# Performance work log

Hardware: AMD Instinct MI355X
Metric: run time of the kernel (lower is better)

## Reference

```python
import jax, jax.numpy as jnp
import numpy as np
from functools import partial

EPS = 1e-5
CHANS = [(3, 64), (64, 64), (64, 128), (128, 128), (128, 256), (256, 256), (256, 256), (256, 256)]

def conv3d(x, w):
    # x: [B,X,Y,Z,Cin], w: [3,3,3,Cin,Cout]; Minkowski stride-1 conv keeps coords -> SAME padding
    return jax.lax.conv_general_dilated(x, w, window_strides=(1, 1, 1), padding='SAME',
                                        dimension_numbers=('NDHWC', 'DHWIO', 'NDHWC'))

def bn(x, g, b):
    # training-mode batch norm over all voxels (MinkowskiBatchNorm forward)
    m = jnp.mean(x, axis=(0, 1, 2, 3))
    v = jnp.var(x, axis=(0, 1, 2, 3))
    return (x - m) * jax.lax.rsqrt(v + EPS) * g + b

def maxpool2(x):
    return jax.lax.reduce_window(x, -jnp.inf, jax.lax.max,
                                 (1, 2, 2, 2, 1), (1, 2, 2, 2, 1), 'VALID')

def setup_inputs() -> dict:
    key = jax.random.key(0)
    ks = jax.random.split(key, 32)
    inp = {'x': jax.random.normal(ks[0], (2, 64, 64, 64, 3), dtype=jnp.float32)}
    for i, (ci, co) in enumerate(CHANS):
        scale = (2.0 / (27 * ci)) ** 0.5  # kaiming for 3x3x3 conv
        inp[f'w{i+1}'] = jax.random.normal(ks[1 + i], (3, 3, 3, ci, co), dtype=jnp.float32) * scale
        inp[f'g{i+1}'] = jnp.ones((co,), dtype=jnp.float32)
        inp[f'b{i+1}'] = jnp.zeros((co,), dtype=jnp.float32)
    inp['wl'] = jax.random.normal(ks[20], (256, 256), dtype=jnp.float32) * (1.0 / 16.0)
    inp['bl'] = jnp.zeros((256,), dtype=jnp.float32)
    return inp

def reference(x, w1, g1, b1, w2, g2, b2, w3, g3, b3, w4, g4, b4,
              w5, g5, b5, w6, g6, b6, w7, g7, b7, w8, g8, b8, wl, bl):
    h = jax.nn.relu(bn(conv3d(x, w1), g1, b1))
    h = jax.nn.relu(bn(conv3d(h, w2), g2, b2))
    h = maxpool2(h)                                   # 64 -> 32
    h = jax.nn.relu(bn(conv3d(h, w3), g3, b3))
    h = jax.nn.relu(bn(conv3d(h, w4), g4, b4))
    h = maxpool2(h)                                   # 32 -> 16
    h = jax.nn.relu(bn(conv3d(h, w5), g5, b5))
    h = jax.nn.relu(bn(conv3d(h, w6), g6, b6))
    h = jax.nn.relu(bn(conv3d(h, w7), g7, b7))
    h = maxpool2(h)                                   # 16 -> 8
    h = bn(conv3d(h, w8), g8, b8)                     # no ReLU before global pool in source
    h = jnp.mean(h, axis=(1, 2, 3))                   # MinkowskiGlobalPooling (avg over coords)
    return h @ wl + bl                                # MinkowskiLinear(256, out_feat)
```

## Files before the change

kernel.cpp:

```cpp
#include <hip/hip_runtime.h>


typedef _Float16 f16;
typedef _Float16 f16x8 __attribute__((ext_vector_type(8)));
typedef _Float16 f16x4 __attribute__((ext_vector_type(4)));
typedef float f32x4 __attribute__((ext_vector_type(4)));

__device__ __forceinline__ int xcd_swz(int bx, int nbx) {
  const int q = nbx >> 3, r = nbx & 7;
  const int x = bx & 7, o = bx >> 3;
  return (x < r ? x * (q + 1) : r * (q + 1) + (x - r) * q) + o;
}

struct WArgs {
  const float* src[8];
  int end[8];
  int S[8], G[8], CR[8], CO[8];
};
__global__ __launch_bounds__(256) void wprep_all(WArgs a, f16* __restrict__ wf)
{
  const int e = blockIdx.x * 256 + threadIdx.x;
  int li = 0;
  while (li < 7 && e >= a.end[li]) ++li;
  if (e >= a.end[li]) return;
  const int base = li ? a.end[li - 1] : 0;
  int x = e - base;
  const int i = x & 7;
  const int l = (x >> 3) & 63;
  int r = x >> 9;
  const int g = r % a.G[li]; r /= a.G[li];
  const int s = r % a.S[li]; r /= a.S[li];
  const int t = r;
  const int k = s * 32 + ((l >> 4) << 3) + i;
  const int co = g * 16 + (l & 15);
  float v;
  if (li == 0) {
    const int tap = k >> 3, ci = k & 7;
    v = (ci < 3 && tap < 27) ? a.src[0][((long)tap * 3 + ci) * 64 + co] : 0.f;
  } else {
    v = (k < a.CR[li]) ? a.src[li][((long)t * a.CR[li] + k) * a.CO[li] + co] : 0.f;
  }
  wf[e] = (f16)v;
}

__global__ __launch_bounds__(256) void conv1_mfma(
    const float* __restrict__ xin, const f16* __restrict__ wf,
    f16* __restrict__ out, float* __restrict__ part)
{
  constexpr int Z = 64, Y = 64, X = 64, L = 4;
  constexpr int RB = 48;
  constexpr int SLAB = (L + 2) * (Z + 2) * RB;
  __shared__ __align__(16) char slab[3 * SLAB];
  __shared__ float sstat[4][2][64];

  const int tid = threadIdx.x;
  const int lane = tid & 63;
  const int wr = tid >> 6;

  const int bxs = xcd_swz(blockIdx.x, gridDim.x);
  const long vb = (long)bxs * 256;
  const int n = (int)(vb >> 18);
  const int rem = (int)(vb & 262143);
  const int x0 = rem >> 12;
  const int y0 = (rem >> 6) & 63;

  if (tid < 36) {
    const int s = tid / 12, pr = tid % 12;
    const int row = (pr >> 1) * (Z + 2) + (pr & 1) * (Z + 1);
    const f16x8 hz = {};
    *(f16x8*)(slab + s * SLAB + row * RB) = hz;
  }

  for (int rr2 = tid; rr2 < 3 * (L + 2) * Z; rr2 += 256) {
    const int s = rr2 / ((L + 2) * Z);
    const int rr = rr2 % ((L + 2) * Z);
    const int li = rr / Z, z = rr % Z;
    const int xs = x0 + s - 1, ys = y0 - 1 + li;
    f16x8 h = {};
    if (xs >= 0 && xs < X && ys >= 0 && ys < Y) {
      const float* p = xin + (((long)(n * X + xs) * Y + ys) * Z + z) * 3;
      h[0] = (f16)p[0]; h[1] = (f16)p[1]; h[2] = (f16)p[2];
    }
    *(f16x8*)(slab + s * SLAB + (li * (Z + 2) + 1 + z) * RB) = h;
  }

  int abase[4];
  #pragma unroll
  for (int r = 0; r < 4; ++r) {
    const int vl = wr * 64 + r * 16 + (lane & 15);
    abase[r] = ((vl >> 6) * (Z + 2) + (vl & 63)) * RB;
  }
  const int c = lane >> 4;
  int rofftab[7];
  #pragma unroll
  for (int j = 0; j < 7; ++j) {
    const int tap = 4 * j + c;
    if (tap < 27) {
      const int dx = tap / 9, dy = (tap / 3) % 3, dz = tap % 3;
      rofftab[j] = dx * SLAB + (dy * (Z + 2) + dz) * RB;
    } else {
      rofftab[j] = 0;
    }
  }

  f32x4 acc[4][4];
  const f32x4 fz = {0.f, 0.f, 0.f, 0.f};
  #pragma unroll
  for (int r = 0; r < 4; ++r)
    #pragma unroll
    for (int cc = 0; cc < 4; ++cc) acc[r][cc] = fz;

  __syncthreads();

  #pragma unroll
  for (int j = 0; j < 7; ++j) {
    f16x8 av[4];
    #pragma unroll
    for (int r = 0; r < 4; ++r)
      av[r] = *(const f16x8*)(slab + abase[r] + rofftab[j]);
    f16x8 bv[4];
    #pragma unroll
    for (int c2 = 0; c2 < 4; ++c2)
      bv[c2] = *(const f16x8*)((const char*)wf + ((j * 4 + c2) << 10) + (lane << 4));
    #pragma unroll
    for (int r = 0; r < 4; ++r)
      #pragma unroll
      for (int c2 = 0; c2 < 4; ++c2)
        acc[r][c2] = __builtin_amdgcn_mfma_f32_16x16x32_f16(av[r], bv[c2], acc[r][c2], 0, 0, 0);
  }

  const long vgbase = vb + wr * 64;
  #pragma unroll
  for (int r = 0; r < 4; ++r)
    #pragma unroll
    for (int cc = 0; cc < 4; ++cc)
      #pragma unroll
      for (int q = 0; q < 4; ++q) {
        const long vox = vgbase + r * 16 + ((lane >> 4) << 2) + q;
        const int co = cc * 16 + (lane & 15);
        out[vox * 64 + co] = (f16)acc[r][cc][q];
      }

  float s4[4], q4[4];
  #pragma unroll
  for (int cc = 0; cc < 4; ++cc) {
    float s = 0.f, q = 0.f;
    #pragma unroll
    for (int r = 0; r < 4; ++r)
      #pragma unroll
      for (int qd = 0; qd < 4; ++qd) {
        const float v = acc[r][cc][qd];
        s += v;
        q = fmaf(v, v, q);
      }
    s4[cc] = s; q4[cc] = q;
  }
  #pragma unroll
  for (int cc = 0; cc < 4; ++cc) {
    s4[cc] += __shfl_xor(s4[cc], 16);
    s4[cc] += __shfl_xor(s4[cc], 32);
    q4[cc] += __shfl_xor(q4[cc], 16);
    q4[cc] += __shfl_xor(q4[cc], 32);
  }
  if (lane < 16) {
    #pragma unroll
    for (int cc = 0; cc < 4; ++cc) {
      sstat[wr][0][cc * 16 + lane] = s4[cc];
      sstat[wr][1][cc * 16 + lane] = q4[cc];
    }
  }
  __syncthreads();
  for (int t = tid; t < 128; t += 256) {
    const int k = (t >> 6) & 1, ch = t & 63;
    float v = 0.f;
    #pragma unroll
    for (int w2 = 0; w2 < 4; ++w2) v += sstat[w2][k][ch];
    part[(long)bxs * 128 + k * 64 + ch] = v;
  }
}

template<int CIN, int Z, int WR, int WC, bool HASBN, int SS>
__global__ __launch_bounds__(WR*WC*64) void conv_mfma(
    const f16* __restrict__ xin, const f16* __restrict__ wf,
    f16* __restrict__ out, int X, int Y, int Co,
    const float* __restrict__ sc, const float* __restrict__ sh,
    float* __restrict__ part, int partBase,
    float* __restrict__ pout, long outE)
{
  constexpr int NTHR = WR * WC * 64;
  constexpr int L = 64 * WR / Z;
  constexpr int RB = CIN * 2;
  constexpr int S = CIN / 32;
  constexpr int COW = 64 * WC;
  constexpr bool SPLIT = (SS > 0);
  __shared__ __align__(16) char slab[(L + 2) * (Z + 2) * RB];
  __shared__ float sstat[SPLIT ? 1 : WR * WC][2][64];

  const int tid = threadIdx.x;
  const int lane = tid & 63;
  const int wv = tid >> 6;
  const int wr = wv / WC, wc = wv % WC;

  const int bxs = xcd_swz(blockIdx.x, gridDim.x);
  const long vb = (long)bxs * (64 * WR);
  const int XYZ = X * Y * Z;
  const int n = (int)(vb / XYZ);
  const int rem = (int)(vb % XYZ);
  const int x0 = rem / (Y * Z);
  const int y0 = (rem % (Y * Z)) / Z;
  const int co0 = blockIdx.y * COW;
  const int Gtot = Co >> 4;
  const int g0 = (co0 >> 4) + wc * 4;

  int arow[4];
  #pragma unroll
  for (int r = 0; r < 4; ++r) {
    const int vl = wr * 64 + r * 16 + (lane & 15);
    arow[r] = (vl / Z) * (Z + 2) + (vl % Z);
  }
  const int kbyte = (lane >> 4) << 4;

  f32x4 acc[4][4];
  const f32x4 fz = {0.f, 0.f, 0.f, 0.f};
  #pragma unroll
  for (int r = 0; r < 4; ++r)
    #pragma unroll
    for (int c = 0; c < 4; ++c) acc[r][c] = fz;

  {
    const f16x8 hz = {};
    for (int e = tid * 8; e < (L + 2) * 2 * CIN; e += NTHR * 8) {
      const int pr = e / CIN, ci = e % CIN;
      const int row = (pr >> 1) * (Z + 2) + (pr & 1) * (Z + 1);
      *(f16x8*)(slab + row * RB + ((ci * 2) ^ ((row & 7) << 4))) = hz;
    }
  }

  auto stage = [&](int dx) {
    const int xs = x0 + dx - 1;
    const bool xok = (xs >= 0) && (xs < X);
    const long gv0 = ((long)(n * X + xs) * Y + (y0 - 1)) * Z;
    constexpr int NE = (L + 2) * Z * CIN;
    for (int e = tid * 8; e < NE; e += NTHR * 8) {
      const int rr = e / CIN, ci = e % CIN;
      const int li = rr / Z, z = rr % Z;
      const int ys = y0 - 1 + li;
      f16x8 h = {};
      if (xok && ys >= 0 && ys < Y) {
        h = *(const f16x8*)(xin + (gv0 + rr) * CIN + ci);
        if constexpr (HASBN) {
          const float4 s0 = *(const float4*)(sc + ci);
          const float4 s1 = *(const float4*)(sc + ci + 4);
          const float4 h0 = *(const float4*)(sh + ci);
          const float4 h1 = *(const float4*)(sh + ci + 4);
          h[0] = (f16)fmaxf(fmaf((float)h[0], s0.x, h0.x), 0.f);
          h[1] = (f16)fmaxf(fmaf((float)h[1], s0.y, h0.y), 0.f);
          h[2] = (f16)fmaxf(fmaf((float)h[2], s0.z, h0.z), 0.f);
          h[3] = (f16)fmaxf(fmaf((float)h[3], s0.w, h0.w), 0.f);
          h[4] = (f16)fmaxf(fmaf((float)h[4], s1.x, h1.x), 0.f);
          h[5] = (f16)fmaxf(fmaf((float)h[5], s1.y, h1.y), 0.f);
          h[6] = (f16)fmaxf(fmaf((float)h[6], s1.z, h1.z), 0.f);
          h[7] = (f16)fmaxf(fmaf((float)h[7], s1.w, h1.w), 0.f);
        }
      }
      const int row = li * (Z + 2) + 1 + z;
      *(f16x8*)(slab + row * RB + ((ci * 2) ^ ((row & 7) << 4))) = h;
    }
  };

  auto ktaps = [&](int dx, int s) {
    #pragma unroll
    for (int dy = 0; dy < 3; ++dy) {
      #pragma unroll
      for (int dzi = 0; dzi < 3; ++dzi) {
        f16x8 av[4];
        #pragma unroll
        for (int r = 0; r < 4; ++r) {
          const int row = arow[r] + dy * (Z + 2) + dzi;
          av[r] = *(const f16x8*)(slab + row * RB +
                    ((s * 64 + kbyte) ^ ((row & 7) << 4)));
        }
        const int t = dx * 9 + dy * 3 + dzi;
        f16x8 bv[4];
        #pragma unroll
        for (int c = 0; c < 4; ++c)
          bv[c] = *(const f16x8*)((const char*)wf +
                    (((long)(t * S + s) * Gtot + g0 + c) << 10) + (lane << 4));
        #pragma unroll
        for (int r = 0; r < 4; ++r)
          #pragma unroll
          for (int c = 0; c < 4; ++c)
            acc[r][c] = __builtin_amdgcn_mfma_f32_16x16x32_f16(av[r], bv[c], acc[r][c], 0, 0, 0);
      }
    }
  };

  if constexpr (SPLIT) {
    constexpr int SCH = S / SS;
    const int zb = blockIdx.z;
    const int dx = zb / SS;
    const int s0 = (zb % SS) * SCH;
    stage(dx);
    __syncthreads();
    #pragma unroll
    for (int si = 0; si < SCH; ++si) ktaps(dx, s0 + si);
  } else {
    for (int dx = 0; dx < 3; ++dx) {
      __syncthreads();
      stage(dx);
      __syncthreads();
      for (int s = 0; s < S; ++s) ktaps(dx, s);
    }
  }

  const long vgbase = vb + wr * 64;
  const int cobase = co0 + wc * 64;
  if constexpr (SPLIT) {
    float* pb = pout + (long)blockIdx.z * outE;
    #pragma unroll
    for (int r = 0; r < 4; ++r)
      #pragma unroll
      for (int c = 0; c < 4; ++c)
        #pragma unroll
        for (int q = 0; q < 4; ++q) {
          const long vox = vgbase + r * 16 + ((lane >> 4) << 2) + q;
          const int co = cobase + c * 16 + (lane & 15);
          pb[vox * Co + co] = acc[r][c][q];
        }
    return;
  }

  #pragma unroll
  for (int r = 0; r < 4; ++r)
    #pragma unroll
    for (int c = 0; c < 4; ++c)
      #pragma unroll
      for (int q = 0; q < 4; ++q) {
        const long vox = vgbase + r * 16 + ((lane >> 4) << 2) + q;
        const int co = cobase + c * 16 + (lane & 15);
        out[vox * Co + co] = (f16)acc[r][c][q];
      }

  float s4[4], q4[4];
  #pragma unroll
  for (int c = 0; c < 4; ++c) {
    float s = 0.f, q = 0.f;
    #pragma unroll
    for (int r = 0; r < 4; ++r)
      #pragma unroll
      for (int qd = 0; qd < 4; ++qd) {
        const float v = acc[r][c][qd];
        s += v;
        q = fmaf(v, v, q);
      }
    s4[c] = s; q4[c] = q;
  }
  #pragma unroll
  for (int c = 0; c < 4; ++c) {
    s4[c] += __shfl_xor(s4[c], 16);
    s4[c] += __shfl_xor(s4[c], 32);
    q4[c] += __shfl_xor(q4[c], 16);
    q4[c] += __shfl_xor(q4[c], 32);
  }
  if (lane < 16) {
    #pragma unroll
    for (int c = 0; c < 4; ++c) {
      sstat[wv][0][c * 16 + lane] = s4[c];
      sstat[wv][1][c * 16 + lane] = q4[c];
    }
  }
  __syncthreads();
  const long entry = (long)blockIdx.y * gridDim.x + bxs + partBase;
  for (int t = tid; t < WC * 128; t += NTHR) {
    const int wcc = t >> 7, k = (t >> 6) & 1, ch = t & 63;
    float v = 0.f;
    #pragma unroll
    for (int wr2 = 0; wr2 < WR; ++wr2) v += sstat[wr2 * WC + wcc][k][ch];
    part[entry * (2 * COW) + k * COW + wcc * 64 + ch] = v;
  }
}

__global__ __launch_bounds__(256) void reduce_stats(
    const float* __restrict__ pout, f16* __restrict__ out,
    long outE, int KS, int vpb, float* __restrict__ part)
{
  const int tid = threadIdx.x;
  const int wv = tid >> 6, lane = tid & 63;
  const int vbase = blockIdx.x * vpb;
  float4 s = {0.f, 0.f, 0.f, 0.f}, q = {0.f, 0.f, 0.f, 0.f};
  for (int v = vbase + wv; v < vbase + vpb; v += 4) {
    const long e = (long)v * 256 + lane * 4;
    float4 o = *(const float4*)(pout + e);
    for (int z = 1; z < KS; ++z) {
      const float4 p = *(const float4*)(pout + (long)z * outE + e);
      o.x += p.x; o.y += p.y; o.z += p.z; o.w += p.w;
    }
    f16x4 ov = {(f16)o.x, (f16)o.y, (f16)o.z, (f16)o.w};
    *(f16x4*)(out + e) = ov;
    s.x += o.x; s.y += o.y; s.z += o.z; s.w += o.w;
    q.x = fmaf(o.x, o.x, q.x); q.y = fmaf(o.y, o.y, q.y);
    q.z = fmaf(o.z, o.z, q.z); q.w = fmaf(o.w, o.w, q.w);
  }
  __shared__ float st[4][2][256];
  *(float4*)&st[wv][0][lane * 4] = s;
  *(float4*)&st[wv][1][lane * 4] = q;
  __syncthreads();
  for (int t = tid; t < 512; t += 256) {
    const int k = t >> 8, ch = t & 255;
    part[(long)blockIdx.x * 512 + k * 256 + ch] =
        st[0][k][ch] + st[1][k][ch] + st[2][k][ch] + st[3][k][ch];
  }
}

__global__ __launch_bounds__(256) void stats_final(
    const float* __restrict__ part, int nbx, int CoWin, long nvox,
    const float* __restrict__ g, const float* __restrict__ b,
    float* __restrict__ sc, float* __restrict__ sh)
{
  const int c = blockIdx.x;
  const int by = c / CoWin;
  const int cw = c % CoWin;
  const int tid = threadIdx.x;
  float s = 0.f, ss = 0.f;
  for (int i = tid; i < nbx; i += 256) {
    const long base = ((long)by * nbx + i) * 2 * CoWin;
    s += part[base + cw];
    ss += part[base + CoWin + cw];
  }
  __shared__ float r0[256];
  __shared__ float r1[256];
  r0[tid] = s; r1[tid] = ss;
  __syncthreads();
  #pragma unroll
  for (int o = 128; o > 0; o >>= 1) {
    if (tid < o) { r0[tid] += r0[tid + o]; r1[tid] += r1[tid + o]; }
    __syncthreads();
  }
  if (tid == 0) {
    const float inv = 1.f / (float)nvox;
    const float m = r0[0] * inv;
    const float var = r1[0] * inv - m * m;
    const float scale = rsqrtf(var + 1e-5f) * g[c];
    sc[c] = scale;
    sh[c] = b[c] - m * scale;
  }
}

__global__ __launch_bounds__(256) void maxpool2_aff(
    const f16* __restrict__ in, f16* __restrict__ out,
    int N, int X, int Y, int Z, int C,
    const float* __restrict__ sc, const float* __restrict__ sh)
{
  const int OX = X >> 1, OY = Y >> 1, OZ = Z >> 1;
  const int c4n = C >> 2;
  const long nout = (long)N * OX * OY * OZ * c4n;
  long idx = (long)blockIdx.x * 256 + threadIdx.x;
  if (idx >= nout) return;
  const int c4 = (int)(idx % c4n);
  long v = idx / c4n;
  const int oz = (int)(v % OZ); v /= OZ;
  const int oy = (int)(v % OY); v /= OY;
  const int ox = (int)(v % OX);
  const int n = (int)(v / OX);
  const long sx = (long)Y * Z * C, sy = (long)Z * C, sz = C;
  const long base = ((((long)n * X + 2 * ox) * Y + 2 * oy) * Z + 2 * oz) * (long)C + 4L * c4;
  f16x4 m = *(const f16x4*)(in + base);
  #pragma unroll
  for (int dd = 1; dd < 8; ++dd) {
    const int dxp = dd >> 2, dyp = (dd >> 1) & 1, dzp = dd & 1;
    const f16x4 t = *(const f16x4*)(in + base + dxp * sx + dyp * sy + dzp * sz);
    #pragma unroll
    for (int i = 0; i < 4; ++i) m[i] = (t[i] > m[i]) ? t[i] : m[i];
  }
  const int c = 4 * c4;
  const float4 s4 = *(const float4*)(sc + c);
  const float4 h4 = *(const float4*)(sh + c);
  f16x4 r;
  r[0] = (f16)fmaxf(fmaf((float)m[0], s4.x, h4.x), 0.f);
  r[1] = (f16)fmaxf(fmaf((float)m[1], s4.y, h4.y), 0.f);
  r[2] = (f16)fmaxf(fmaf((float)m[2], s4.z, h4.z), 0.f);
  r[3] = (f16)fmaxf(fmaf((float)m[3], s4.w, h4.w), 0.f);
  *(f16x4*)(out + idx * 4) = r;
}

__global__ __launch_bounds__(256) void head_mean(
    const f16* __restrict__ x8, const float* __restrict__ sc, const float* __restrict__ sh,
    float* __restrict__ hbuf)
{
  const int n = blockIdx.x, cg = blockIdx.y;
  const int tx = threadIdx.x & 63, ty = threadIdx.x >> 6;
  const int c = cg * 64 + tx;
  float s = 0.f;
  for (int v = ty; v < 512; v += 4) s += (float)x8[((long)n * 512 + v) * 256 + c];
  __shared__ float red[4][64];
  red[ty][tx] = s;
  __syncthreads();
  if (ty == 0) {
    s = red[0][tx] + red[1][tx] + red[2][tx] + red[3][tx];
    hbuf[n * 256 + c] = fmaf(s * (1.f / 512.f), sc[c], sh[c]);
  }
}

__global__ __launch_bounds__(256) void head_mv(
    const float* __restrict__ hbuf, const float* __restrict__ wl,
    const float* __restrict__ bl, float* __restrict__ out)
{
  const int n = blockIdx.x, og = blockIdx.y;
  const int tx = threadIdx.x & 63, ty = threadIdx.x >> 6;
  const int oc = og * 64 + tx;
  float a = 0.f;
  const int k0 = ty * 64;
  for (int k = k0; k < k0 + 64; ++k)
    a = fmaf(hbuf[n * 256 + k], wl[(long)k * 256 + oc], a);
  __shared__ float red[4][64];
  red[ty][tx] = a;
  __syncthreads();
  if (ty == 0)
    out[n * 256 + oc] = red[0][tx] + red[1][tx] + red[2][tx] + red[3][tx] + bl[oc];
}

extern "C" void kernel_launch(void* const* d_in, const int* in_sizes, int n_in,
                              void* d_out, int out_size, void* d_ws, size_t ws_size,
                              hipStream_t stream)
{
  const float* x = (const float*)d_in[0];
  const float* W[8];
  const float* G[8];
  const float* B[8];
  for (int i = 0; i < 8; ++i) {
    W[i] = (const float*)d_in[1 + 3 * i];
    G[i] = (const float*)d_in[2 + 3 * i];
    B[i] = (const float*)d_in[3 + 3 * i];
  }
  const float* wl = (const float*)d_in[25];
  const float* bl = (const float*)d_in[26];

  char* ws = (char*)d_ws;
  f16*   A    = (f16*)ws;
  f16*   Bb   = (f16*)(ws + (64L << 20));
  float* pK   = (float*)(ws + (128L << 20));
  float* part = (float*)(ws + (152L << 20));
  float* scb  = part + 262144L;
  float* shb  = scb + 2048L;
  float* hbuf = shb + 2048L;
  f16*   wfb  = (f16*)(hbuf + 512L);

  const int wfS[8]  = {7, 2, 2, 4, 4, 8, 8, 8};
  const int wfG[8]  = {4, 4, 8, 8, 16, 16, 16, 16};
  const int wfT[8]  = {1, 27, 27, 27, 27, 27, 27, 27};
  const int wfCR[8] = {3, 64, 64, 128, 128, 256, 256, 256};
  const int wfCO[8] = {64, 64, 128, 128, 256, 256, 256, 256};
  long wfOff[9];
  wfOff[0] = 0;
  for (int i = 0; i < 8; ++i) wfOff[i + 1] = wfOff[i] + (long)wfT[i] * wfS[i] * wfG[i] * 512;
  if (ws_size < (size_t)((char*)(wfb + wfOff[8]) - ws)) return;
  auto WF = [&](int i) { return wfb + wfOff[i]; };
  auto SC = [&](int i) { return scb + i * 256; };
  auto SH = [&](int i) { return shb + i * 256; };

  {
    WArgs a;
    for (int i = 0; i < 8; ++i) {
      a.src[i] = W[i]; a.end[i] = (int)wfOff[i + 1];
      a.S[i] = wfS[i]; a.G[i] = wfG[i]; a.CR[i] = wfCR[i]; a.CO[i] = wfCO[i];
    }
    wprep_all<<<(unsigned)((wfOff[8] + 255) / 256), 256, 0, stream>>>(a, wfb);
  }

  auto fin = [&](int layer, int nbx, int CoWin, int C, long nvox) {
    stats_final<<<C, 256, 0, stream>>>(part, nbx, CoWin, nvox,
                                       G[layer], B[layer], SC(layer), SH(layer));
  };
  auto pool_aff = [&](const f16* in, f16* ob, int N, int Xd, int Yd, int Zd, int C, int layer) {
    const long nout = (long)N * (Xd / 2) * (Yd / 2) * (Zd / 2) * (C / 4);
    maxpool2_aff<<<(unsigned)((nout + 255) / 256), 256, 0, stream>>>(
        in, ob, N, Xd, Yd, Zd, C, SC(layer), SH(layer));
  };

  conv1_mfma<<<2048, 256, 0, stream>>>(x, WF(0), A, part);
  fin(0, 2048, 64, 64, 524288);
  conv_mfma<64, 64, 4, 1, true, 0><<<dim3(2048, 1), 256, 0, stream>>>(
      A, WF(1), Bb, 64, 64, 64, SC(0), SH(0), part, 0, nullptr, 0);
  fin(1, 2048, 64, 64, 524288);
  pool_aff(Bb, A, 2, 64, 64, 64, 64, 1);

  conv_mfma<64, 32, 2, 2, false, 0><<<dim3(512, 1), 256, 0, stream>>>(
      A, WF(2), Bb, 32, 32, 128, nullptr, nullptr, part, 0, nullptr, 0);
  fin(2, 512, 128, 128, 65536);
  conv_mfma<128, 32, 2, 2, true, 0><<<dim3(512, 1), 256, 0, stream>>>(
      Bb, WF(3), A, 32, 32, 128, SC(2), SH(2), part, 0, nullptr, 0);
  fin(3, 512, 128, 128, 65536);
  pool_aff(A, Bb, 2, 32, 32, 32, 128, 3);

  const long E16 = 2097152;
  conv_mfma<128, 16, 1, 4, false, 1><<<dim3(128, 1, 3), 256, 0, stream>>>(
      Bb, WF(4), nullptr, 16, 16, 256, nullptr, nullptr, nullptr, 0, pK, E16);
  reduce_stats<<<256, 256, 0, stream>>>(pK, A, E16, 3, 32, part);
  fin(4, 256, 256, 256, 8192);
  conv_mfma<256, 16, 1, 4, true, 1><<<dim3(128, 1, 3), 256, 0, stream>>>(
      A, WF(5), nullptr, 16, 16, 256, SC(4), SH(4), nullptr, 0, pK, E16);
  reduce_stats<<<256, 256, 0, stream>>>(pK, Bb, E16, 3, 32, part);
  fin(5, 256, 256, 256, 8192);
  conv_mfma<256, 16, 1, 4, true, 1><<<dim3(128, 1, 3), 256, 0, stream>>>(
      Bb, WF(6), nullptr, 16, 16, 256, SC(5), SH(5), nullptr, 0, pK, E16);
  reduce_stats<<<256, 256, 0, stream>>>(pK, A, E16, 3, 32, part);
  fin(6, 256, 256, 256, 8192);
  pool_aff(A, Bb, 2, 16, 16, 16, 256, 6);

  const long E8 = 262144;
  conv_mfma<256, 8, 1, 4, false, 4><<<dim3(16, 1, 12), 256, 0, stream>>>(
      Bb, WF(7), nullptr, 8, 8, 256, nullptr, nullptr, nullptr, 0, pK, E8);
  reduce_stats<<<256, 256, 0, stream>>>(pK, A, E8, 12, 4, part);
  fin(7, 256, 256, 256, 1024);

  head_mean<<<dim3(2, 4), 256, 0, stream>>>(A, SC(7), SH(7), hbuf);
  head_mv<<<dim3(2, 4), 256, 0, stream>>>(hbuf, wl, bl, (float*)d_out);
}
```

Measured before the change: 572.1 us.

## Add double-buffered z-half pipelined conv kernel for non-split layers

Adds a conv_pipe kernel that splits each dx slab into two z-halves, double-buffers them in shared memory, and prefetches the next stage into registers while MFMAs run on the current one. Global loads now overlap with compute instead of serialising behind a barrier between stage and compute. It is used for conv2, conv3 and conv4, and the old conv_mfma is reduced to the split-K path. The cost is more barriers (six stages instead of three), extra halo rows per half, and register pressure from the prefetch buffers.

Result: slower. 728.9 us (+27.4%).

```diff
diff --git a/kernel.cpp b/kernel.cpp
--- a/kernel.cpp
+++ b/kernel.cpp
@@ -179,22 +179,27 @@
   }
 }
 
-template<int CIN, int Z, int WR, int WC, bool HASBN, int SS>
-__global__ __launch_bounds__(WR*WC*64) void conv_mfma(
+template<int CIN, int Z, int WR, int WC, bool HASBN>
+__global__ __launch_bounds__(WR*WC*64) void conv_pipe(
     const f16* __restrict__ xin, const f16* __restrict__ wf,
     f16* __restrict__ out, int X, int Y, int Co,
     const float* __restrict__ sc, const float* __restrict__ sh,
-    float* __restrict__ part, int partBase,
-    float* __restrict__ pout, long outE)
+    float* __restrict__ part, int partBase)
 {
   constexpr int NTHR = WR * WC * 64;
   constexpr int L = 64 * WR / Z;
-  constexpr int RB = CIN * 2;
+  constexpr int ZH = Z / 2;
+  constexpr int ZR = ZH + 2;
+  constexpr int RBB = CIN * 2;
+  constexpr int HROWS = (L + 2) * ZR;
+  constexpr int NE_H = HROWS * CIN;
+  constexpr int NLD = (NE_H + NTHR * 8 - 1) / (NTHR * 8);
+  constexpr int NL2 = (NLD + 1) / 2;
   constexpr int S = CIN / 32;
+  constexpr int SH2 = S / 2;
   constexpr int COW = 64 * WC;
-  constexpr bool SPLIT = (SS > 0);
-  __shared__ __align__(16) char slab[(L + 2) * (Z + 2) * RB];
-  __shared__ float sstat[SPLIT ? 1 : WR * WC][2][64];
+  __shared__ __align__(16) char slab[2][HROWS * RBB];
+  __shared__ float sstat[WR * WC][2][64];
 
   const int tid = threadIdx.x;
   const int lane = tid & 63;
@@ -216,6 +221,209 @@
   #pragma unroll
   for (int r = 0; r < 4; ++r) {
     const int vl = wr * 64 + r * 16 + (lane & 15);
+    arow[r] = (vl / Z) * ZR + ((r * 16) % ZH) + (lane & 15);
+  }
+  const int kbyte = (lane >> 4) << 4;
+
+  f32x4 acc[4][4];
+  const f32x4 fz = {0.f, 0.f, 0.f, 0.f};
+  #pragma unroll
+  for (int r = 0; r < 4; ++r)
+    #pragma unroll
+    for (int c = 0; c < 4; ++c) acc[r][c] = fz;
+
+  f16x8 regs[NL2];
+
+  auto LOADH = [&](int k1, int half) {
+    const int dx = k1 >> 1, zh = k1 & 1;
+    const int xs = x0 + dx - 1;
+    const long gplane = (long)(n * X + xs) * Y;
+    #pragma unroll
+    for (int j = 0; j < NL2; ++j) {
+      const int slot = half * NL2 + j;
+      const int e = tid * 8 + slot * NTHR * 8;
+      f16x8 h = {};
+      if (slot < NLD && e < NE_H) {
+        const int rr = e / CIN, ci = e % CIN;
+        const int li = rr / ZR, zr = rr % ZR;
+        const int ys = y0 - 1 + li;
+        const int zs = zh * ZH - 1 + zr;
+        if (xs >= 0 && xs < X && ys >= 0 && ys < Y && zs >= 0 && zs < Z)
+          h = *(const f16x8*)(xin + ((gplane + ys) * Z + zs) * CIN + ci);
+      }
+      regs[j] = h;
+    }
+  };
+
+  auto WRITEH = [&](int k1, int half) {
+    const int dx = k1 >> 1, zh = k1 & 1;
+    const int xs = x0 + dx - 1;
+    char* buf = slab[k1 & 1];
+    #pragma unroll
+    for (int j = 0; j < NL2; ++j) {
+      const int slot = half * NL2 + j;
+      const int e = tid * 8 + slot * NTHR * 8;
+      if (slot < NLD && e < NE_H) {
+        const int rr = e / CIN, ci = e % CIN;
+        const int li = rr / ZR, zr = rr % ZR;
+        const int ys = y0 - 1 + li;
+        const int zs = zh * ZH - 1 + zr;
+        f16x8 h = regs[j];
+        if constexpr (HASBN) {
+          if (xs >= 0 && xs < X && ys >= 0 && ys < Y && zs >= 0 && zs < Z) {
+            const float4 s0 = *(const float4*)(sc + ci);
+            const float4 s1 = *(const float4*)(sc + ci + 4);
+            const float4 h0 = *(const float4*)(sh + ci);
+            const float4 h1 = *(const float4*)(sh + ci + 4);
+            h[0] = (f16)fmaxf(fmaf((float)h[0], s0.x, h0.x), 0.f);
+            h[1] = (f16)fmaxf(fmaf((float)h[1], s0.y, h0.y), 0.f);
+            h[2] = (f16)fmaxf(fmaf((float)h[2], s0.z, h0.z), 0.f);
+            h[3] = (f16)fmaxf(fmaf((float)h[3], s0.w, h0.w), 0.f);
+            h[4] = (f16)fmaxf(fmaf((float)h[4], s1.x, h1.x), 0.f);
+            h[5] = (f16)fmaxf(fmaf((float)h[5], s1.y, h1.y), 0.f);
+            h[6] = (f16)fmaxf(fmaf((float)h[6], s1.z, h1.z), 0.f);
+            h[7] = (f16)fmaxf(fmaf((float)h[7], s1.w, h1.w), 0.f);
+          }
+        }
+        *(f16x8*)(buf + rr * RBB + ((ci * 2) ^ ((rr & 7) << 4))) = h;
+      }
+    }
+  };
+
+  auto ktaps = [&](int k, int s) {
+    const int dx = k >> 1, zh = k & 1;
+    const char* buf = slab[k & 1];
+    #pragma unroll
+    for (int dy = 0; dy < 3; ++dy) {
+      #pragma unroll
+      for (int dzi = 0; dzi < 3; ++dzi) {
+        f16x8 av[4];
+        #pragma unroll
+        for (int r = 0; r < 4; ++r) {
+          if (((r * 16) % Z) / ZH == zh) {
+            const int row = arow[r] + dy * ZR + dzi;
+            av[r] = *(const f16x8*)(buf + row * RBB +
+                      ((s * 64 + kbyte) ^ ((row & 7) << 4)));
+          }
+        }
+        const int t = dx * 9 + dy * 3 + dzi;
+        f16x8 bv[4];
+        #pragma unroll
+        for (int c = 0; c < 4; ++c)
+          bv[c] = *(const f16x8*)((const char*)wf +
+                    (((long)(t * S + s) * Gtot + g0 + c) << 10) + (lane << 4));
+        #pragma unroll
+        for (int r = 0; r < 4; ++r) {
+          if (((r * 16) % Z) / ZH == zh) {
+            #pragma unroll
+            for (int c = 0; c < 4; ++c)
+              acc[r][c] = __builtin_amdgcn_mfma_f32_16x16x32_f16(av[r], bv[c], acc[r][c], 0, 0, 0);
+          }
+        }
+      }
+    }
+  };
+
+  LOADH(0, 0); WRITEH(0, 0);
+  LOADH(0, 1); WRITEH(0, 1);
+  __syncthreads();
+
+  for (int k = 0; k < 6; ++k) {
+    if (k < 5) LOADH(k + 1, 0);
+    for (int si = 0; si < SH2; ++si) ktaps(k, si);
+    if (k < 5) WRITEH(k + 1, 0);
+    if (k < 5) LOADH(k + 1, 1);
+    for (int si = SH2; si < S; ++si) ktaps(k, si);
+    if (k < 5) WRITEH(k + 1, 1);
+    __syncthreads();
+  }
+
+  const long vgbase = vb + wr * 64;
+  const int cobase = co0 + wc * 64;
+  #pragma unroll
+  for (int r = 0; r < 4; ++r)
+    #pragma unroll
+    for (int c = 0; c < 4; ++c)
+      #pragma unroll
+      for (int q = 0; q < 4; ++q) {
+        const long vox = vgbase + r * 16 + ((lane >> 4) << 2) + q;
+        const int co = cobase + c * 16 + (lane & 15);
+        out[vox * Co + co] = (f16)acc[r][c][q];
+      }
+
+  float s4[4], q4[4];
+  #pragma unroll
+  for (int c = 0; c < 4; ++c) {
+    float s = 0.f, q = 0.f;
+    #pragma unroll
+    for (int r = 0; r < 4; ++r)
+      #pragma unroll
+      for (int qd = 0; qd < 4; ++qd) {
+        const float v = acc[r][c][qd];
+        s += v;
+        q = fmaf(v, v, q);
+      }
+    s4[c] = s; q4[c] = q;
+  }
+  #pragma unroll
+  for (int c = 0; c < 4; ++c) {
+    s4[c] += __shfl_xor(s4[c], 16);
+    s4[c] += __shfl_xor(s4[c], 32);
+    q4[c] += __shfl_xor(q4[c], 16);
+    q4[c] += __shfl_xor(q4[c], 32);
+  }
+  if (lane < 16) {
+    #pragma unroll
+    for (int c = 0; c < 4; ++c) {
+      sstat[wv][0][c * 16 + lane] = s4[c];
+      sstat[wv][1][c * 16 + lane] = q4[c];
+    }
+  }
+  __syncthreads();
+  const long entry = (long)blockIdx.y * gridDim.x + bxs + partBase;
+  for (int t = tid; t < WC * 128; t += NTHR) {
+    const int wcc = t >> 7, k = (t >> 6) & 1, ch = t & 63;
+    float v = 0.f;
+    #pragma unroll
+    for (int wr2 = 0; wr2 < WR; ++wr2) v += sstat[wr2 * WC + wcc][k][ch];
+    part[entry * (2 * COW) + k * COW + wcc * 64 + ch] = v;
+  }
+}
+
+template<int CIN, int Z, int WR, int WC, bool HASBN, int SS>
+__global__ __launch_bounds__(WR*WC*64) void conv_mfma(
+    const f16* __restrict__ xin, const f16* __restrict__ wf,
+    f16* __restrict__ out, int X, int Y, int Co,
+    const float* __restrict__ sc, const float* __restrict__ sh,
+    float* __restrict__ part, int partBase,
+    float* __restrict__ pout, long outE)
+{
+  constexpr int NTHR = WR * WC * 64;
+  constexpr int L = 64 * WR / Z;
+  constexpr int RB = CIN * 2;
+  constexpr int S = CIN / 32;
+  __shared__ __align__(16) char slab[(L + 2) * (Z + 2) * RB];
+
+  const int tid = threadIdx.x;
+  const int lane = tid & 63;
+  const int wv = tid >> 6;
+  const int wr = wv / WC, wc = wv % WC;
+
+  const int bxs = xcd_swz(blockIdx.x, gridDim.x);
+  const long vb = (long)bxs * (64 * WR);
+  const int XYZ = X * Y * Z;
+  const int n = (int)(vb / XYZ);
+  const int rem = (int)(vb % XYZ);
+  const int x0 = rem / (Y * Z);
+  const int y0 = (rem % (Y * Z)) / Z;
+  const int co0 = blockIdx.y * (64 * WC);
+  const int Gtot = Co >> 4;
+  const int g0 = (co0 >> 4) + wc * 4;
+
+  int arow[4];
+  #pragma unroll
+  for (int r = 0; r < 4; ++r) {
+    const int vl = wr * 64 + r * 16 + (lane & 15);
     arow[r] = (vl / Z) * (Z + 2) + (vl % Z);
   }
   const int kbyte = (lane >> 4) << 4;
@@ -236,7 +444,10 @@
     }
   }
 
-  auto stage = [&](int dx) {
+  const int zb = blockIdx.z;
+  const int dx = zb / SS;
+  const int s0 = (zb % SS) * (S / SS);
+  {
     const int xs = x0 + dx - 1;
     const bool xok = (xs >= 0) && (xs < X);
     const long gv0 = ((long)(n * X + xs) * Y + (y0 - 1)) * Z;
@@ -249,26 +460,28 @@
       if (xok && ys >= 0 && ys < Y) {
         h = *(const f16x8*)(xin + (gv0 + rr) * CIN + ci);
         if constexpr (HASBN) {
-          const float4 s0 = *(const float4*)(sc + ci);
-          const float4 s1 = *(const float4*)(sc + ci + 4);
-          const float4 h0 = *(const float4*)(sh + ci);
-          const float4 h1 = *(const float4*)(sh + ci + 4);
-          h[0] = (f16)fmaxf(fmaf((float)h[0], s0.x, h0.x), 0.f);
-          h[1] = (f16)fmaxf(fmaf((float)h[1], s0.y, h0.y), 0.f);
-          h[2] = (f16)fmaxf(fmaf((float)h[2], s0.z, h0.z), 0.f);
-          h[3] = (f16)fmaxf(fmaf((float)h[3], s0.w, h0.w), 0.f);
-          h[4] = (f16)fmaxf(fmaf((float)h[4], s1.x, h1.x), 0.f);
-          h[5] = (f16)fmaxf(fmaf((float)h[5], s1.y, h1.y), 0.f);
-          h[6] = (f16)fmaxf(fmaf((float)h[6], s1.z, h1.z), 0.f);
-          h[7] = (f16)fmaxf(fmaf((float)h[7], s1.w, h1.w), 0.f);
+          const float4 sc0 = *(const float4*)(sc + ci);
+          const float4 sc1 = *(const float4*)(sc + ci + 4);
+          const float4 sh0 = *(const float4*)(sh + ci);
+          const float4 sh1 = *(const float4*)(sh + ci + 4);
+          h[0] = (f16)fmaxf(fmaf((float)h[0], sc0.x, sh0.x), 0.f);
+          h[1] = (f16)fmaxf(fmaf((float)h[1], sc0.y, sh0.y), 0.f);
+          h[2] = (f16)fmaxf(fmaf((float)h[2], sc0.z, sh0.z), 0.f);
+          h[3] = (f16)fmaxf(fmaf((float)h[3], sc0.w, sh0.w), 0.f);
+          h[4] = (f16)fmaxf(fmaf((float)h[4], sc1.x, sh1.x), 0.f);
+          h[5] = (f16)fmaxf(fmaf((float)h[5], sc1.y, sh1.y), 0.f);
+          h[6] = (f16)fmaxf(fmaf((float)h[6], sc1.z, sh1.z), 0.f);
+          h[7] = (f16)fmaxf(fmaf((float)h[7], sc1.w, sh1.w), 0.f);
         }
       }
       const int row = li * (Z + 2) + 1 + z;
       *(f16x8*)(slab + row * RB + ((ci * 2) ^ ((row & 7) << 4))) = h;
     }
-  };
-
-  auto ktaps = [&](int dx, int s) {
+  }
+  __syncthreads();
+
+  for (int si = 0; si < S / SS; ++si) {
+    const int s = s0 + si;
     #pragma unroll
     for (int dy = 0; dy < 3; ++dy) {
       #pragma unroll
@@ -293,43 +506,11 @@
             acc[r][c] = __builtin_amdgcn_mfma_f32_16x16x32_f16(av[r], bv[c], acc[r][c], 0, 0, 0);
       }
     }
-  };
-
-  if constexpr (SPLIT) {
-    constexpr int SCH = S / SS;
-    const int zb = blockIdx.z;
-    const int dx = zb / SS;
-    const int s0 = (zb % SS) * SCH;
-    stage(dx);
-    __syncthreads();
-    #pragma unroll
-    for (int si = 0; si < SCH; ++si) ktaps(dx, s0 + si);
-  } else {
-    for (int dx = 0; dx < 3; ++dx) {
-      __syncthreads();
-      stage(dx);
-      __syncthreads();
-      for (int s = 0; s < S; ++s) ktaps(dx, s);
-    }
   }
 
   const long vgbase = vb + wr * 64;
   const int cobase = co0 + wc * 64;
-  if constexpr (SPLIT) {
-    float* pb = pout + (long)blockIdx.z * outE;
-    #pragma unroll
-    for (int r = 0; r < 4; ++r)
-      #pragma unroll
-      for (int c = 0; c < 4; ++c)
-        #pragma unroll
-        for (int q = 0; q < 4; ++q) {
-          const long vox = vgbase + r * 16 + ((lane >> 4) << 2) + q;
-          const int co = cobase + c * 16 + (lane & 15);
-          pb[vox * Co + co] = acc[r][c][q];
-        }
-    return;
-  }
-
+  float* pb = pout + (long)blockIdx.z * outE;
   #pragma unroll
   for (int r = 0; r < 4; ++r)
     #pragma unroll
@@ -338,46 +519,8 @@
       for (int q = 0; q < 4; ++q) {
         const long vox = vgbase + r * 16 + ((lane >> 4) << 2) + q;
         const int co = cobase + c * 16 + (lane & 15);
-        out[vox * Co + co] = (f16)acc[r][c][q];
-      }
-
-  float s4[4], q4[4];
-  #pragma unroll
-  for (int c = 0; c < 4; ++c) {
-    float s = 0.f, q = 0.f;
-    #pragma unroll
-    for (int r = 0; r < 4; ++r)
-      #pragma unroll
-      for (int qd = 0; qd < 4; ++qd) {
-        const float v = acc[r][c][qd];
-        s += v;
-        q = fmaf(v, v, q);
-      }
-    s4[c] = s; q4[c] = q;
-  }
-  #pragma unroll
-  for (int c = 0; c < 4; ++c) {
-    s4[c] += __shfl_xor(s4[c], 16);
-    s4[c] += __shfl_xor(s4[c], 32);
-    q4[c] += __shfl_xor(q4[c], 16);
-    q4[c] += __shfl_xor(q4[c], 32);
-  }
-  if (lane < 16) {
-    #pragma unroll
-    for (int c = 0; c < 4; ++c) {
-      sstat[wv][0][c * 16 + lane] = s4[c];
-      sstat[wv][1][c * 16 + lane] = q4[c];
-    }
-  }
-  __syncthreads();
-  const long entry = (long)blockIdx.y * gridDim.x + bxs + partBase;
-  for (int t = tid; t < WC * 128; t += NTHR) {
-    const int wcc = t >> 7, k = (t >> 6) & 1, ch = t & 63;
-    float v = 0.f;
-    #pragma unroll
-    for (int wr2 = 0; wr2 < WR; ++wr2) v += sstat[wr2 * WC + wcc][k][ch];
-    part[entry * (2 * COW) + k * COW + wcc * 64 + ch] = v;
-  }
+        pb[vox * Co + co] = acc[r][c][q];
+      }
 }
 
 __global__ __launch_bounds__(256) void reduce_stats(
@@ -579,16 +722,16 @@
 
   conv1_mfma<<<2048, 256, 0, stream>>>(x, WF(0), A, part);
   fin(0, 2048, 64, 64, 524288);
-  conv_mfma<64, 64, 4, 1, true, 0><<<dim3(2048, 1), 256, 0, stream>>>(
-      A, WF(1), Bb, 64, 64, 64, SC(0), SH(0), part, 0, nullptr, 0);
+  conv_pipe<64, 64, 4, 1, true><<<dim3(2048, 1), 256, 0, stream>>>(
+      A, WF(1), Bb, 64, 64, 64, SC(0), SH(0), part, 0);
   fin(1, 2048, 64, 64, 524288);
   pool_aff(Bb, A, 2, 64, 64, 64, 64, 1);
 
-  conv_mfma<64, 32, 2, 2, false, 0><<<dim3(512, 1), 256, 0, stream>>>(
-      A, WF(2), Bb, 32, 32, 128, nullptr, nullptr, part, 0, nullptr, 0);
+  conv_pipe<64, 32, 2, 2, false><<<dim3(512, 1), 256, 0, stream>>>(
+      A, WF(2), Bb, 32, 32, 128, nullptr, nullptr, part, 0);
   fin(2, 512, 128, 128, 65536);
-  conv_mfma<128, 32, 2, 2, true, 0><<<dim3(512, 1), 256, 0, stream>>>(
-      Bb, WF(3), A, 32, 32, 128, SC(2), SH(2), part, 0, nullptr, 0);
+  conv_pipe<128, 32, 2, 2, true><<<dim3(512, 1), 256, 0, stream>>>(
+      Bb, WF(3), A, 32, 32, 128, SC(2), SH(2), part, 0);
   fin(3, 512, 128, 128, 65536);
   pool_aff(A, Bb, 2, 32, 32, 32, 128, 3);
 
```

## Pre-pad BN'd conv2 input and stream slabs via direct global-to-LDS loads

Applied to the files above, without the earlier changes.

Adds a bnpad kernel that applies layer-1 BN+ReLU and writes a zero-padded 66^3 fp16 tensor, then a dedicated conv2 kernel that fills its LDS slab with global_load_lds DMA instead of per-thread guarded loads with inline affine. Separately, the generic conv kernel drops the XOR swizzle in favour of row padding (CIN+8) and precomputed A base offsets. The aim is to cut address math and register traffic in staging and LDS fetches. The cost is an extra full pass writing the padded tensor to memory plus an extra launch.

Result: no change. 578.4 us (+1.1%).

```diff
diff --git a/kernel.cpp b/kernel.cpp
--- a/kernel.cpp
+++ b/kernel.cpp
@@ -1,4 +1,5 @@
 #include <hip/hip_runtime.h>
+#include <stdint.h>
 
 
 typedef _Float16 f16;
@@ -179,6 +180,168 @@
   }
 }
 
+__global__ __launch_bounds__(256) void bnpad(
+    const f16* __restrict__ in, f16* __restrict__ outp,
+    const float* __restrict__ sc, const float* __restrict__ sh)
+{
+  const long NT = 2L * 66 * 66 * 66 * 8;
+  long idx = (long)blockIdx.x * 256 + threadIdx.x;
+  if (idx >= NT) return;
+  const int c8 = (int)(idx & 7);
+  long v = idx >> 3;
+  const int zp = (int)(v % 66); v /= 66;
+  const int yp = (int)(v % 66); v /= 66;
+  const int xp = (int)(v % 66);
+  const int n = (int)(v / 66);
+  f16x8 h = {};
+  if (xp >= 1 && xp <= 64 && yp >= 1 && yp <= 64 && zp >= 1 && zp <= 64) {
+    const long src = ((((long)n * 64 + xp - 1) * 64 + yp - 1) * 64 + zp - 1) * 64 + c8 * 8;
+    h = *(const f16x8*)(in + src);
+    const int ci = c8 * 8;
+    const float4 s0 = *(const float4*)(sc + ci);
+    const float4 s1 = *(const float4*)(sc + ci + 4);
+    const float4 h0 = *(const float4*)(sh + ci);
+    const float4 h1 = *(const float4*)(sh + ci + 4);
+    h[0] = (f16)fmaxf(fmaf((float)h[0], s0.x, h0.x), 0.f);
+    h[1] = (f16)fmaxf(fmaf((float)h[1], s0.y, h0.y), 0.f);
+    h[2] = (f16)fmaxf(fmaf((float)h[2], s0.z, h0.z), 0.f);
+    h[3] = (f16)fmaxf(fmaf((float)h[3], s0.w, h0.w), 0.f);
+    h[4] = (f16)fmaxf(fmaf((float)h[4], s1.x, h1.x), 0.f);
+    h[5] = (f16)fmaxf(fmaf((float)h[5], s1.y, h1.y), 0.f);
+    h[6] = (f16)fmaxf(fmaf((float)h[6], s1.z, h1.z), 0.f);
+    h[7] = (f16)fmaxf(fmaf((float)h[7], s1.w, h1.w), 0.f);
+  }
+  *(f16x8*)(outp + idx * 8) = h;
+}
+
+__global__ __launch_bounds__(256) void conv2_dma(
+    const f16* __restrict__ xp, const f16* __restrict__ wf,
+    f16* __restrict__ out, float* __restrict__ part)
+{
+  constexpr int ZP = 66;
+  constexpr int RB = 128;
+  constexpr int SLABB = 51200;
+  __shared__ __align__(1024) char slab[SLABB];
+  __shared__ float sstat[4][2][64];
+
+  const int tid = threadIdx.x;
+  const int lane = tid & 63;
+  const int wv = tid >> 6;
+
+  const int bxs = xcd_swz(blockIdx.x, gridDim.x);
+  const long vb = (long)bxs * 256;
+  const int n = (int)(vb >> 18);
+  const int rem = (int)(vb & 262143);
+  const int x0 = rem >> 12;
+  const int y0 = (rem >> 6) & 63;
+
+  const int srcoff = ((lane >> 3) << 7) | ((((lane & 7) ^ ((lane >> 3) & 7))) << 4);
+
+  int arow[4];
+  #pragma unroll
+  for (int r = 0; r < 4; ++r) {
+    const int vl = wv * 64 + r * 16 + (lane & 15);
+    arow[r] = (vl >> 6) * ZP + (vl & 63);
+  }
+  const int kbyte = (lane >> 4) << 4;
+
+  f32x4 acc[4][4];
+  const f32x4 fz = {0.f, 0.f, 0.f, 0.f};
+  #pragma unroll
+  for (int r = 0; r < 4; ++r)
+    #pragma unroll
+    for (int c = 0; c < 4; ++c) acc[r][c] = fz;
+
+  for (int dx = 0; dx < 3; ++dx) {
+    __syncthreads();
+    const char* gsrc = (const char*)xp +
+        (((long)(n * 66 + (x0 + dx)) * 66 + y0) * (long)(ZP * 64 * 2));
+    for (int i = wv; i < 50; i += 4) {
+      __builtin_amdgcn_global_load_lds(
+          (const __attribute__((address_space(1))) uint32_t*)(const void*)(gsrc + (long)i * 1024 + srcoff),
+          (__attribute__((address_space(3))) uint32_t*)(void*)(slab + i * 1024),
+          16, 0, 0);
+    }
+    __syncthreads();
+
+    for (int s = 0; s < 2; ++s) {
+      #pragma unroll
+      for (int dy = 0; dy < 3; ++dy) {
+        #pragma unroll
+        for (int dzi = 0; dzi < 3; ++dzi) {
+          f16x8 av[4];
+          #pragma unroll
+          for (int r = 0; r < 4; ++r) {
+            const int row = arow[r] + dy * ZP + dzi;
+            av[r] = *(const f16x8*)(slab + row * RB +
+                      ((s * 64 + kbyte) ^ ((row & 7) << 4)));
+          }
+          const int t = dx * 9 + dy * 3 + dzi;
+          f16x8 bv[4];
+          #pragma unroll
+          for (int c = 0; c < 4; ++c)
+            bv[c] = *(const f16x8*)((const char*)wf +
+                      (((long)(t * 2 + s) * 4 + c) << 10) + (lane << 4));
+          #pragma unroll
+          for (int r = 0; r < 4; ++r)
+            #pragma unroll
+            for (int c = 0; c < 4; ++c)
+              acc[r][c] = __builtin_amdgcn_mfma_f32_16x16x32_f16(av[r], bv[c], acc[r][c], 0, 0, 0);
+        }
+      }
+    }
+  }
+
+  const long vgbase = vb + wv * 64;
+  #pragma unroll
+  for (int r = 0; r < 4; ++r)
+    #pragma unroll
+    for (int c = 0; c < 4; ++c)
+      #pragma unroll
+      for (int q = 0; q < 4; ++q) {
+        const long vox = vgbase + r * 16 + ((lane >> 4) << 2) + q;
+        const int co = c * 16 + (lane & 15);
+        out[vox * 64 + co] = (f16)acc[r][c][q];
+      }
+
+  float s4[4], q4[4];
+  #pragma unroll
+  for (int c = 0; c < 4; ++c) {
+    float s = 0.f, q = 0.f;
+    #pragma unroll
+    for (int r = 0; r < 4; ++r)
+      #pragma unroll
+      for (int qd = 0; qd < 4; ++qd) {
+        const float v = acc[r][c][qd];
+        s += v;
+        q = fmaf(v, v, q);
+      }
+    s4[c] = s; q4[c] = q;
+  }
+  #pragma unroll
+  for (int c = 0; c < 4; ++c) {
+    s4[c] += __shfl_xor(s4[c], 16);
+    s4[c] += __shfl_xor(s4[c], 32);
+    q4[c] += __shfl_xor(q4[c], 16);
+    q4[c] += __shfl_xor(q4[c], 32);
+  }
+  if (lane < 16) {
+    #pragma unroll
+    for (int c = 0; c < 4; ++c) {
+      sstat[wv][0][c * 16 + lane] = s4[c];
+      sstat[wv][1][c * 16 + lane] = q4[c];
+    }
+  }
+  __syncthreads();
+  for (int t = tid; t < 128; t += 256) {
+    const int k = (t >> 6) & 1, ch = t & 63;
+    float v = 0.f;
+    #pragma unroll
+    for (int w2 = 0; w2 < 4; ++w2) v += sstat[w2][k][ch];
+    part[(long)bxs * 128 + k * 64 + ch] = v;
+  }
+}
+
 template<int CIN, int Z, int WR, int WC, bool HASBN, int SS>
 __global__ __launch_bounds__(WR*WC*64) void conv_mfma(
     const f16* __restrict__ xin, const f16* __restrict__ wf,
@@ -189,7 +352,7 @@
 {
   constexpr int NTHR = WR * WC * 64;
   constexpr int L = 64 * WR / Z;
-  constexpr int RB = CIN * 2;
+  constexpr int RB = (CIN + 8) * 2;
   constexpr int S = CIN / 32;
   constexpr int COW = 64 * WC;
   constexpr bool SPLIT = (SS > 0);
@@ -212,13 +375,12 @@
   const int Gtot = Co >> 4;
   const int g0 = (co0 >> 4) + wc * 4;
 
-  int arow[4];
+  int abase[4];
   #pragma unroll
   for (int r = 0; r < 4; ++r) {
     const int vl = wr * 64 + r * 16 + (lane & 15);
-    arow[r] = (vl / Z) * (Z + 2) + (vl % Z);
-  }
-  const int kbyte = (lane >> 4) << 4;
+    abase[r] = ((vl / Z) * (Z + 2) + (vl % Z)) * RB + ((lane >> 4) << 4);
+  }
 
   f32x4 acc[4][4];
   const f32x4 fz = {0.f, 0.f, 0.f, 0.f};
@@ -232,7 +394,7 @@
     for (int e = tid * 8; e < (L + 2) * 2 * CIN; e += NTHR * 8) {
       const int pr = e / CIN, ci = e % CIN;
       const int row = (pr >> 1) * (Z + 2) + (pr & 1) * (Z + 1);
-      *(f16x8*)(slab + row * RB + ((ci * 2) ^ ((row & 7) << 4))) = hz;
+      *(f16x8*)(slab + row * RB + ci * 2) = hz;
     }
   }
 
@@ -263,8 +425,7 @@
           h[7] = (f16)fmaxf(fmaf((float)h[7], s1.w, h1.w), 0.f);
         }
       }
-      const int row = li * (Z + 2) + 1 + z;
-      *(f16x8*)(slab + row * RB + ((ci * 2) ^ ((row & 7) << 4))) = h;
+      *(f16x8*)(slab + (li * (Z + 2) + 1 + z) * RB + ci * 2) = h;
     }
   };
 
@@ -275,11 +436,8 @@
       for (int dzi = 0; dzi < 3; ++dzi) {
         f16x8 av[4];
         #pragma unroll
-        for (int r = 0; r < 4; ++r) {
-          const int row = arow[r] + dy * (Z + 2) + dzi;
-          av[r] = *(const f16x8*)(slab + row * RB +
-                    ((s * 64 + kbyte) ^ ((row & 7) << 4)));
-        }
+        for (int r = 0; r < 4; ++r)
+          av[r] = *(const f16x8*)(slab + abase[r] + s * 64 + (dy * (Z + 2) + dzi) * RB);
         const int t = dx * 9 + dy * 3 + dzi;
         f16x8 bv[4];
         #pragma unroll
@@ -538,8 +696,9 @@
   char* ws = (char*)d_ws;
   f16*   A    = (f16*)ws;
   f16*   Bb   = (f16*)(ws + (64L << 20));
+  f16*   P1   = (f16*)(ws + (128L << 20));
   float* pK   = (float*)(ws + (128L << 20));
-  float* part = (float*)(ws + (152L << 20));
+  float* part = (float*)(ws + (204L << 20));
   float* scb  = part + 262144L;
   float* shb  = scb + 2048L;
   float* hbuf = shb + 2048L;
@@ -579,8 +738,11 @@
 
   conv1_mfma<<<2048, 256, 0, stream>>>(x, WF(0), A, part);
   fin(0, 2048, 64, 64, 524288);
-  conv_mfma<64, 64, 4, 1, true, 0><<<dim3(2048, 1), 256, 0, stream>>>(
-      A, WF(1), Bb, 64, 64, 64, SC(0), SH(0), part, 0, nullptr, 0);
+  {
+    const long NT = 2L * 66 * 66 * 66 * 8;
+    bnpad<<<(unsigned)((NT + 255) / 256), 256, 0, stream>>>(A, P1, SC(0), SH(0));
+  }
+  conv2_dma<<<2048, 256, 0, stream>>>(P1, WF(1), Bb, part);
   fin(1, 2048, 64, 64, 524288);
   pool_aff(Bb, A, 2, 64, 64, 64, 64, 1);
 
```
